# Kernel tuning notes

Hardware: AMD Instinct MI355X
Metric: run time of the kernel (lower is better)

Reference implementation:

```python
import jax, jax.numpy as jnp
import numpy as np

B, S, D = 1, 2048, 2048
H, KVH, HD = 32, 8, 64  # head_dim = D // H
THETA = 10000.0
INIT_STD = 0.02


def _freqs_cos_sin(head_dim, end, theta):
    # precompute_freqs_cis, returned as (cos, sin) real tables [end, head_dim//2]
    freqs = 1.0 / theta ** (np.arange(0, head_dim, 2)[: head_dim // 2].astype(np.float32) / head_dim)
    t = np.arange(end)
    fr = np.outer(t, freqs).astype(np.float32)
    return jnp.asarray(np.cos(fr)), jnp.asarray(np.sin(fr))


def setup_inputs() -> dict:
    key = jax.random.key(0)
    ks = jax.random.split(key, 5)
    return {
        "hidden_states": jax.random.normal(ks[0], (B, S, D), jnp.float32),
        "wq": jax.random.normal(ks[1], (D, H * HD), jnp.float32) * INIT_STD,
        "wk": jax.random.normal(ks[2], (D, KVH * HD), jnp.float32) * INIT_STD,
        "wv": jax.random.normal(ks[3], (D, KVH * HD), jnp.float32) * INIT_STD,
        "wo": jax.random.normal(ks[4], (H * HD, D), jnp.float32) * INIT_STD,
        "position_ids": jnp.broadcast_to(jnp.arange(S, dtype=jnp.int32), (B, S)),
    }


def reference(hidden_states, wq, wk, wv, wo, position_ids):
    # QKV projections (no bias)
    xq = (hidden_states @ wq).reshape(B, S, H, HD)
    xk = (hidden_states @ wk).reshape(B, S, KVH, HD)
    xv = (hidden_states @ wv).reshape(B, S, KVH, HD)

    # rotary embedding: interleaved complex pairs over last dim
    cos_t, sin_t = _freqs_cos_sin(HD, S, THETA)        # [S, HD//2]
    cos = cos_t[position_ids][:, :, None, :]            # [B, S, 1, HD//2]
    sin = sin_t[position_ids][:, :, None, :]

    def rope(x):
        xr = x.astype(jnp.float32).reshape(*x.shape[:-1], -1, 2)
        a, b = xr[..., 0], xr[..., 1]
        # (a + i b) * (cos + i sin)
        ra = a * cos - b * sin
        rb = a * sin + b * cos
        return jnp.stack((ra, rb), axis=-1).reshape(x.shape)

    xq = rope(xq)
    xk = rope(xk)

    # GQA: repeat kv heads
    n_rep = H // KVH
    xk = jnp.repeat(xk[:, :, :, None, :], n_rep, axis=3).reshape(B, S, H, HD)
    xv = jnp.repeat(xv[:, :, :, None, :], n_rep, axis=3).reshape(B, S, H, HD)

    # causal masked softmax attention (full score matrix, as in dot_product_attention_weights)
    scores = jnp.einsum('bqhd,bkhd->bhqk', xq, xk) / np.float32(np.sqrt(HD))
    causal = jnp.tril(jnp.ones((S, S), dtype=bool))
    big_neg = jnp.finfo(jnp.float32).min
    scores = jnp.where(causal[None, None, :, :], scores, big_neg)
    attn = jax.nn.softmax(scores, axis=-1)

    out = jnp.einsum('bhqk,bkhd->bqhd', attn, xv).reshape(B, S, H * HD)
    return out @ wo
```

## Files before the change

kernel.cpp:

```cpp
#include <hip/hip_runtime.h>
#include <hip/hip_bf16.h>


using short8  = __attribute__((ext_vector_type(8))) short;
using f32x4   = __attribute__((ext_vector_type(4))) float;
using f32x16  = __attribute__((ext_vector_type(16))) float;
using f32x2   = __attribute__((ext_vector_type(2))) float;
using ushort4v= __attribute__((ext_vector_type(4))) unsigned short;

#define SEQ 2048
#define DIM 2048
#define NH  32
#define NKVH 8
#define HD  64
#define KVD 512
#define NQKV 3072

#define GLOAD_LDS16(g, l) \
  __builtin_amdgcn_global_load_lds((const __attribute__((address_space(1))) void*)(g), \
                                   (__attribute__((address_space(3))) void*)(l), 16, 0, 0)

__device__ __forceinline__ float bf2f(unsigned short u) {
  union { float f; unsigned v; } x; x.v = ((unsigned)u) << 16; return x.f;
}
__device__ __forceinline__ unsigned short f2bf(float f) {
  union { float f; unsigned v; } x; x.f = f;
  unsigned r = x.v + 0x7fffu + ((x.v >> 16) & 1u);
  return (unsigned short)(r >> 16);
}

__global__ __launch_bounds__(256) void k_cast(const float* __restrict__ src,
                                              unsigned short* __restrict__ dst, int n) {
  int idx = (blockIdx.x * 256 + threadIdx.x) * 4;
  if (idx < n) {
    f32x4 v = *(const f32x4*)(src + idx);
    ushort4v o;
    o[0] = f2bf(v[0]); o[1] = f2bf(v[1]); o[2] = f2bf(v[2]); o[3] = f2bf(v[3]);
    *(ushort4v*)(dst + idx) = o;
  }
}

__global__ __launch_bounds__(256) void k_tcast(const float* __restrict__ src, int C,
                                               unsigned short* __restrict__ dst) {
  __shared__ float tile[32][33];
  int c0 = blockIdx.x * 32, r0 = blockIdx.y * 32;
  int tx = threadIdx.x, ty = threadIdx.y;
  #pragma unroll
  for (int j = 0; j < 32; j += 8)
    tile[ty + j][tx] = src[(r0 + ty + j) * C + c0 + tx];
  __syncthreads();
  #pragma unroll
  for (int j = 0; j < 32; j += 8)
    dst[(c0 + ty + j) * 2048 + r0 + tx] = f2bf(tile[tx][ty + j]);
}

__global__ __launch_bounds__(256) void k_table(const int* __restrict__ pos,
                                               f32x2* __restrict__ tab) {
  int i = blockIdx.x * 256 + threadIdx.x;
  int s = i >> 5, p = i & 31;
  float freq = powf(10000.0f, -(float)(2 * p) / 64.0f);
  float ang = (float)pos[s] * freq;
  float sv, cv; sincosf(ang, &sv, &cv);
  f32x2 r; r[0] = cv; r[1] = sv;
  tab[i] = r;
}

template <int N, bool OUTF32>
__global__ __launch_bounds__(256) void k_gemm(const unsigned short* __restrict__ A,
                                              const unsigned short* __restrict__ Bt,
                                              void* __restrict__ Cout) {
  const int K = 2048;
  __shared__ unsigned short lA[128 * 64];
  __shared__ unsigned short lB[128 * 64];
  int m0 = blockIdx.y * 128, n0 = blockIdx.x * 128;
  int t = threadIdx.x, lane = t & 63, wid = t >> 6;
  int wr = wid >> 1, wc = wid & 1;
  int lr = lane & 15, lg = lane >> 4;

  f32x4 acc[4][4] = {};

  for (int k0 = 0; k0 < K; k0 += 64) {
    #pragma unroll
    for (int j = 0; j < 4; ++j) {
      int idx = t + 256 * j, row = idx >> 3, c8 = idx & 7;
      GLOAD_LDS16(A  + (m0 + row) * K + k0 + c8 * 8, lA + idx * 8);
      GLOAD_LDS16(Bt + (n0 + row) * K + k0 + c8 * 8, lB + idx * 8);
    }
    __syncthreads();
    #pragma unroll
    for (int kk = 0; kk < 64; kk += 32) {
      short8 af[4], bfr[4];
      #pragma unroll
      for (int i = 0; i < 4; ++i) {
        af[i]  = *(const short8*)(lA + (wr * 64 + i * 16 + lr) * 64 + kk + lg * 8);
        bfr[i] = *(const short8*)(lB + (wc * 64 + i * 16 + lr) * 64 + kk + lg * 8);
      }
      #pragma unroll
      for (int i = 0; i < 4; ++i)
        #pragma unroll
        for (int j = 0; j < 4; ++j)
          acc[i][j] = __builtin_amdgcn_mfma_f32_16x16x32_bf16(af[i], bfr[j], acc[i][j], 0, 0, 0);
    }
    __syncthreads();
  }
  #pragma unroll
  for (int i = 0; i < 4; ++i)
    #pragma unroll
    for (int j = 0; j < 4; ++j)
      #pragma unroll
      for (int r = 0; r < 4; ++r) {
        int row = m0 + wr * 64 + i * 16 + lg * 4 + r;
        int col = n0 + wc * 64 + j * 16 + lr;
        float v = acc[i][j][r];
        if constexpr (OUTF32) ((float*)Cout)[row * N + col] = v;
        else ((unsigned short*)Cout)[row * N + col] = f2bf(v);
      }
}

__global__ __launch_bounds__(256) void k_rope(const unsigned short* __restrict__ xqkv,
                                              const f32x2* __restrict__ tab,
                                              unsigned short* __restrict__ xq,
                                              unsigned short* __restrict__ xk) {
  int s = blockIdx.y;
  int j = blockIdx.x * 256 + threadIdx.x;
  bool isq = j < 1024;
  int col = isq ? (2 * j) : (DIM + 2 * (j - 1024));
  int p = (col >> 1) & 31;
  f32x2 cs = tab[s * 32 + p];
  unsigned both = *(const unsigned*)(xqkv + s * NQKV + col);
  float a = bf2f((unsigned short)(both & 0xffff));
  float b = bf2f((unsigned short)(both >> 16));
  float ra = a * cs[0] - b * cs[1];
  float rb = a * cs[1] + b * cs[0];
  if (isq) { ra *= 0.125f; rb *= 0.125f; }
  unsigned pk = (unsigned)f2bf(ra) | ((unsigned)f2bf(rb) << 16);
  if (isq) *(unsigned*)(xq + s * DIM + col) = pk;
  else     *(unsigned*)(xk + s * KVD + (col - DIM)) = pk;
}

__global__ __launch_bounds__(256) void k_vt(const unsigned short* __restrict__ xqkv,
                                            unsigned short* __restrict__ xvT) {
  __shared__ unsigned short tile[32][33];
  int c0 = blockIdx.x * 32, s0 = blockIdx.y * 32;
  int tx = threadIdx.x, ty = threadIdx.y;
  #pragma unroll
  for (int j = 0; j < 32; j += 8)
    tile[ty + j][tx] = xqkv[(s0 + ty + j) * NQKV + 2560 + c0 + tx];
  __syncthreads();
  #pragma unroll
  for (int j = 0; j < 32; j += 8)
    xvT[(c0 + ty + j) * SEQ + s0 + tx] = tile[tx][ty + j];
}

__global__ __launch_bounds__(256) void k_attn(const unsigned short* __restrict__ xq,
                                              const unsigned short* __restrict__ xk,
                                              const unsigned short* __restrict__ xvT,
                                              unsigned short* __restrict__ attnout) {
  int wid = threadIdx.x >> 6, lane = threadIdx.x & 63;
  int tid = blockIdx.x * 4 + wid;
  int h = tid >> 5, j = tid & 31;
  int kvh = h >> 2;
  int lq = lane & 31, hi = lane >> 5;

  #pragma unroll
  for (int ph = 0; ph < 2; ++ph) {
    int qb = ph ? (63 - j) : j;
    int q0 = qb * 32;

    short8 qf[4];
    #pragma unroll
    for (int s = 0; s < 4; ++s)
      qf[s] = *(const short8*)(xq + (q0 + lq) * DIM + h * HD + s * 16 + hi * 8);

    f32x16 o0 = {}, o1 = {};
    float m = -3.0e38f, l = 0.0f;

    for (int kv0 = 0; kv0 <= q0; kv0 += 32) {
      f32x16 st = {};
      #pragma unroll
      for (int s = 0; s < 4; ++s) {
        short8 kf = *(const short8*)(xk + (kv0 + lq) * KVD + kvh * HD + s * 16 + hi * 8);
        st = __builtin_amdgcn_mfma_f32_32x32x16_bf16(kf, qf[s], st, 0, 0, 0);
      }
      if (kv0 == q0) {
        #pragma unroll
        for (int r = 0; r < 16; ++r) {
          int kvl = (r & 3) + 8 * (r >> 2) + 4 * hi;
          if (kvl > lq) st[r] = -3.0e38f;
        }
      }
      float pmax = st[0];
      #pragma unroll
      for (int r = 1; r < 16; ++r) pmax = fmaxf(pmax, st[r]);
      pmax = fmaxf(pmax, __shfl_xor(pmax, 32));
      if (!__all(pmax - m <= 8.0f)) {
        float mnew = fmaxf(m, pmax);
        float scale = __expf(m - mnew);
        #pragma unroll
        for (int r = 0; r < 16; ++r) {
          int ql = (r & 3) + 8 * (r >> 2) + 4 * hi;
          float sc = __shfl(scale, ql);
          o0[r] *= sc; o1[r] *= sc;
        }
        l *= scale;
        m = mnew;
      }
      float p[16], sum = 0.0f;
      #pragma unroll
      for (int r = 0; r < 16; ++r) { p[r] = __expf(st[r] - m); sum += p[r]; }
      l += sum;
      unsigned w[8];
      #pragma unroll
      for (int i = 0; i < 8; ++i)
        asm("v_cvt_pk_bf16_f32 %0, %1, %2" : "=v"(w[i]) : "v"(p[2 * i]), "v"(p[2 * i + 1]));
      #pragma unroll
      for (int s2 = 0; s2 < 2; ++s2) {
        int b = s2 * 4;
        unsigned sw0 = __shfl_xor(w[b + 0], 32);
        unsigned sw1 = __shfl_xor(w[b + 1], 32);
        unsigned sw2 = __shfl_xor(w[b + 2], 32);
        unsigned sw3 = __shfl_xor(w[b + 3], 32);
        union { unsigned u[4]; short8 s8; } pa;
        pa.u[0] = hi ? sw2 : w[b + 0];
        pa.u[1] = hi ? sw3 : w[b + 1];
        pa.u[2] = hi ? w[b + 2] : sw0;
        pa.u[3] = hi ? w[b + 3] : sw1;
        short8 v0 = *(const short8*)(xvT + (kvh * HD + lq)      * SEQ + kv0 + s2 * 16 + hi * 8);
        short8 v1 = *(const short8*)(xvT + (kvh * HD + 32 + lq) * SEQ + kv0 + s2 * 16 + hi * 8);
        o0 = __builtin_amdgcn_mfma_f32_32x32x16_bf16(pa.s8, v0, o0, 0, 0, 0);
        o1 = __builtin_amdgcn_mfma_f32_32x32x16_bf16(pa.s8, v1, o1, 0, 0, 0);
      }
    }
    float lt = l + __shfl_xor(l, 32);
    float linv = 1.0f / lt;
    #pragma unroll
    for (int r = 0; r < 16; ++r) {
      int ql = (r & 3) + 8 * (r >> 2) + 4 * hi;
      float li = __shfl(linv, ql);
      int row = q0 + ql;
      attnout[row * DIM + h * HD + lq]      = f2bf(o0[r] * li);
      attnout[row * DIM + h * HD + 32 + lq] = f2bf(o1[r] * li);
    }
  }
}

extern "C" void kernel_launch(void* const* d_in, const int* in_sizes, int n_in,
                              void* d_out, int out_size, void* d_ws, size_t ws_size,
                              hipStream_t stream) {
  const float* hs = (const float*)d_in[0];
  const float* wq = (const float*)d_in[1];
  const float* wk = (const float*)d_in[2];
  const float* wv = (const float*)d_in[3];
  const float* wo = (const float*)d_in[4];
  const int* pos  = (const int*)d_in[5];
  float* out = (float*)d_out;

  char* ws = (char*)d_ws;
  unsigned short* wqkvT = (unsigned short*)(ws);
  unsigned short* woT   = (unsigned short*)(ws + 12582912);
  unsigned short* hbf   = (unsigned short*)(ws + 20971520);
  unsigned short* xqkv  = (unsigned short*)(ws + 29360128);
  unsigned short* xq    = (unsigned short*)(ws + 41943040);
  unsigned short* xk    = (unsigned short*)(ws + 50331648);
  unsigned short* xvT   = (unsigned short*)(ws + 52428800);
  f32x2*          tab   = (f32x2*)(ws + 54525952);
  unsigned short* attnout = hbf;

  k_cast<<<4096, 256, 0, stream>>>(hs, hbf, SEQ * DIM);
  k_tcast<<<dim3(64, 64), dim3(32, 8), 0, stream>>>(wq, 2048, wqkvT);
  k_tcast<<<dim3(16, 64), dim3(32, 8), 0, stream>>>(wk, 512, wqkvT + 2048 * 2048);
  k_tcast<<<dim3(16, 64), dim3(32, 8), 0, stream>>>(wv, 512, wqkvT + 2560 * 2048);
  k_tcast<<<dim3(64, 64), dim3(32, 8), 0, stream>>>(wo, 2048, woT);
  k_table<<<256, 256, 0, stream>>>(pos, tab);

  k_gemm<NQKV, false><<<dim3(NQKV / 128, SEQ / 128), 256, 0, stream>>>(hbf, wqkvT, xqkv);

  k_rope<<<dim3(5, SEQ), 256, 0, stream>>>(xqkv, tab, xq, xk);
  k_vt<<<dim3(16, 64), dim3(32, 8), 0, stream>>>(xqkv, xvT);

  k_attn<<<256, 256, 0, stream>>>(xq, xk, xvT, attnout);

  k_gemm<DIM, true><<<dim3(DIM / 128, SEQ / 128), 256, 0, stream>>>(attnout, woT, out);
}
```

Measured before the change: 296.0 us.

## Split attention KV range across two wave halves and merge partial softmax states

The attention kernel now runs 512 threads per block. Each block holds the four query heads that share one KV head, and the causal KV range is split between two groups of waves, with the partial max, sum and output merged through shared memory. It also software-prefetches the next K/V tile into registers, raises wave priority around the MFMA sections, and folds log2(e) into the Q scale so the kernel can use exp2 directly. The intent is to double the waves per block to hide latency and shorten the critical path of long causal rows, at the cost of extra registers, shared-memory merge work and block-level syncs.

```diff
diff --git a/kernel.cpp b/kernel.cpp
--- a/kernel.cpp
+++ b/kernel.cpp
@@ -132,7 +132,8 @@
   float b = bf2f((unsigned short)(both >> 16));
   float ra = a * cs[0] - b * cs[1];
   float rb = a * cs[1] + b * cs[0];
-  if (isq) { ra *= 0.125f; rb *= 0.125f; }
+  const float QS = 0.125f * 1.44269504088896f;
+  if (isq) { ra *= QS; rb *= QS; }
   unsigned pk = (unsigned)f2bf(ra) | ((unsigned)f2bf(rb) << 16);
   if (isq) *(unsigned*)(xq + s * DIM + col) = pk;
   else     *(unsigned*)(xk + s * KVD + (col - DIM)) = pk;
@@ -152,20 +153,41 @@
     xvT[(c0 + ty + j) * SEQ + s0 + tx] = tile[tx][ty + j];
 }
 
-__global__ __launch_bounds__(256) void k_attn(const unsigned short* __restrict__ xq,
+__global__ __launch_bounds__(512) void k_attn(const unsigned short* __restrict__ xq,
                                               const unsigned short* __restrict__ xk,
                                               const unsigned short* __restrict__ xvT,
                                               unsigned short* __restrict__ attnout) {
+  __shared__ float obuf[4][64 * 36];
+  __shared__ float sm_m[4][2][32];
+  __shared__ float sm_l[4][32];
+
   int wid = threadIdx.x >> 6, lane = threadIdx.x & 63;
-  int tid = blockIdx.x * 4 + wid;
-  int h = tid >> 5, j = tid & 31;
-  int kvh = h >> 2;
+  int kvh = blockIdx.x & 7, j = blockIdx.x >> 3;
+  int h3 = wid & 3, half = wid >> 2;
+  int h = kvh * 4 + h3;
   int lq = lane & 31, hi = lane >> 5;
 
-  #pragma unroll
+  auto loadK = [&](int kv0, short8* d) {
+    #pragma unroll
+    for (int s = 0; s < 4; ++s)
+      d[s] = *(const short8*)(xk + (kv0 + lq) * KVD + kvh * HD + s * 16 + hi * 8);
+  };
+  auto loadV = [&](int kv0, short8* d) {
+    #pragma unroll
+    for (int s2 = 0; s2 < 2; ++s2) {
+      d[s2 * 2 + 0] = *(const short8*)(xvT + (kvh * HD + lq)      * SEQ + kv0 + s2 * 16 + hi * 8);
+      d[s2 * 2 + 1] = *(const short8*)(xvT + (kvh * HD + 32 + lq) * SEQ + kv0 + s2 * 16 + hi * 8);
+    }
+  };
+
+  #pragma unroll 1
   for (int ph = 0; ph < 2; ++ph) {
     int qb = ph ? (63 - j) : j;
     int q0 = qb * 32;
+    int T = qb + 1;
+    int c0 = (T + 1) >> 1;
+    int t0 = half ? c0 : 0;
+    int t1 = half ? T : c0;
 
     short8 qf[4];
     #pragma unroll
@@ -175,72 +197,110 @@
     f32x16 o0 = {}, o1 = {};
     float m = -3.0e38f, l = 0.0f;
 
-    for (int kv0 = 0; kv0 <= q0; kv0 += 32) {
-      f32x16 st = {};
-      #pragma unroll
-      for (int s = 0; s < 4; ++s) {
-        short8 kf = *(const short8*)(xk + (kv0 + lq) * KVD + kvh * HD + s * 16 + hi * 8);
-        st = __builtin_amdgcn_mfma_f32_32x32x16_bf16(kf, qf[s], st, 0, 0, 0);
-      }
-      if (kv0 == q0) {
-        #pragma unroll
-        for (int r = 0; r < 16; ++r) {
-          int kvl = (r & 3) + 8 * (r >> 2) + 4 * hi;
-          if (kvl > lq) st[r] = -3.0e38f;
+    if (t0 < t1) {
+      short8 kf[4], vf[4];
+      loadK(t0 * 32, kf); loadV(t0 * 32, vf);
+
+      for (int t = t0; t < t1; ++t) {
+        int kv0 = t * 32;
+        int kvn = min(t + 1, t1 - 1) * 32;
+        short8 kn[4], vn[4];
+        loadK(kvn, kn); loadV(kvn, vn);
+
+        f32x16 st = {};
+        __builtin_amdgcn_s_setprio(1);
+        #pragma unroll
+        for (int s = 0; s < 4; ++s)
+          st = __builtin_amdgcn_mfma_f32_32x32x16_bf16(kf[s], qf[s], st, 0, 0, 0);
+        __builtin_amdgcn_s_setprio(0);
+
+        if (kv0 == q0) {
+          #pragma unroll
+          for (int r = 0; r < 16; ++r) {
+            int kvl = (r & 3) + 8 * (r >> 2) + 4 * hi;
+            if (kvl > lq) st[r] = -3.0e38f;
+          }
         }
-      }
-      float pmax = st[0];
-      #pragma unroll
-      for (int r = 1; r < 16; ++r) pmax = fmaxf(pmax, st[r]);
-      pmax = fmaxf(pmax, __shfl_xor(pmax, 32));
-      if (!__all(pmax - m <= 8.0f)) {
-        float mnew = fmaxf(m, pmax);
-        float scale = __expf(m - mnew);
-        #pragma unroll
-        for (int r = 0; r < 16; ++r) {
-          int ql = (r & 3) + 8 * (r >> 2) + 4 * hi;
-          float sc = __shfl(scale, ql);
-          o0[r] *= sc; o1[r] *= sc;
+        float pmax = st[0];
+        #pragma unroll
+        for (int r = 1; r < 16; ++r) pmax = fmaxf(pmax, st[r]);
+        pmax = fmaxf(pmax, __shfl_xor(pmax, 32));
+        if (!__all(pmax - m <= 11.54f)) {
+          float mnew = fmaxf(m, pmax);
+          float scale = exp2f(m - mnew);
+          #pragma unroll
+          for (int r = 0; r < 16; ++r) {
+            int ql = (r & 3) + 8 * (r >> 2) + 4 * hi;
+            float sc = __shfl(scale, ql);
+            o0[r] *= sc; o1[r] *= sc;
+          }
+          l *= scale;
+          m = mnew;
         }
-        l *= scale;
-        m = mnew;
-      }
-      float p[16], sum = 0.0f;
-      #pragma unroll
-      for (int r = 0; r < 16; ++r) { p[r] = __expf(st[r] - m); sum += p[r]; }
-      l += sum;
-      unsigned w[8];
-      #pragma unroll
-      for (int i = 0; i < 8; ++i)
-        asm("v_cvt_pk_bf16_f32 %0, %1, %2" : "=v"(w[i]) : "v"(p[2 * i]), "v"(p[2 * i + 1]));
-      #pragma unroll
-      for (int s2 = 0; s2 < 2; ++s2) {
-        int b = s2 * 4;
-        unsigned sw0 = __shfl_xor(w[b + 0], 32);
-        unsigned sw1 = __shfl_xor(w[b + 1], 32);
-        unsigned sw2 = __shfl_xor(w[b + 2], 32);
-        unsigned sw3 = __shfl_xor(w[b + 3], 32);
-        union { unsigned u[4]; short8 s8; } pa;
-        pa.u[0] = hi ? sw2 : w[b + 0];
-        pa.u[1] = hi ? sw3 : w[b + 1];
-        pa.u[2] = hi ? w[b + 2] : sw0;
-        pa.u[3] = hi ? w[b + 3] : sw1;
-        short8 v0 = *(const short8*)(xvT + (kvh * HD + lq)      * SEQ + kv0 + s2 * 16 + hi * 8);
-        short8 v1 = *(const short8*)(xvT + (kvh * HD + 32 + lq) * SEQ + kv0 + s2 * 16 + hi * 8);
-        o0 = __builtin_amdgcn_mfma_f32_32x32x16_bf16(pa.s8, v0, o0, 0, 0, 0);
-        o1 = __builtin_amdgcn_mfma_f32_32x32x16_bf16(pa.s8, v1, o1, 0, 0, 0);
-      }
-    }
-    float lt = l + __shfl_xor(l, 32);
-    float linv = 1.0f / lt;
-    #pragma unroll
-    for (int r = 0; r < 16; ++r) {
-      int ql = (r & 3) + 8 * (r >> 2) + 4 * hi;
-      float li = __shfl(linv, ql);
-      int row = q0 + ql;
-      attnout[row * DIM + h * HD + lq]      = f2bf(o0[r] * li);
-      attnout[row * DIM + h * HD + 32 + lq] = f2bf(o1[r] * li);
-    }
+        float p[16], sum = 0.0f;
+        #pragma unroll
+        for (int r = 0; r < 16; ++r) { p[r] = exp2f(st[r] - m); sum += p[r]; }
+        l += sum;
+        unsigned w[8];
+        #pragma unroll
+        for (int i = 0; i < 8; ++i)
+          asm("v_cvt_pk_bf16_f32 %0, %1, %2" : "=v"(w[i]) : "v"(p[2 * i]), "v"(p[2 * i + 1]));
+        __builtin_amdgcn_s_setprio(1);
+        #pragma unroll
+        for (int s2 = 0; s2 < 2; ++s2) {
+          int b = s2 * 4;
+          unsigned sw0 = __shfl_xor(w[b + 0], 32);
+          unsigned sw1 = __shfl_xor(w[b + 1], 32);
+          unsigned sw2 = __shfl_xor(w[b + 2], 32);
+          unsigned sw3 = __shfl_xor(w[b + 3], 32);
+          union { unsigned u[4]; short8 s8; } pa;
+          pa.u[0] = hi ? sw2 : w[b + 0];
+          pa.u[1] = hi ? sw3 : w[b + 1];
+          pa.u[2] = hi ? w[b + 2] : sw0;
+          pa.u[3] = hi ? w[b + 3] : sw1;
+          o0 = __builtin_amdgcn_mfma_f32_32x32x16_bf16(pa.s8, vf[s2 * 2 + 0], o0, 0, 0, 0);
+          o1 = __builtin_amdgcn_mfma_f32_32x32x16_bf16(pa.s8, vf[s2 * 2 + 1], o1, 0, 0, 0);
+        }
+        __builtin_amdgcn_s_setprio(0);
+        #pragma unroll
+        for (int s = 0; s < 4; ++s) { kf[s] = kn[s]; vf[s] = vn[s]; }
+      }
+    }
+
+    float lc = l + __shfl_xor(l, 32);
+    if (hi == 0) sm_m[h3][half][lq] = m;
+    __syncthreads();
+    float mo = sm_m[h3][half ^ 1][lq];
+    float mstar = fmaxf(m, mo);
+    float s = exp2f(m - mstar);
+    if (half) {
+      if (hi == 0) sm_l[h3][lq] = lc * s;
+      float* ob = &obuf[h3][lane * 36];
+      #pragma unroll
+      for (int r = 0; r < 16; ++r) {
+        int ql = (r & 3) + 8 * (r >> 2) + 4 * hi;
+        float sc = __shfl(s, ql);
+        ob[r] = o0[r] * sc;
+        ob[16 + r] = o1[r] * sc;
+      }
+    }
+    __syncthreads();
+    if (!half) {
+      float lB = sm_l[h3][lq];
+      float ltot = lc * s + lB;
+      float linv = 1.0f / ltot;
+      const float* ob = &obuf[h3][lane * 36];
+      #pragma unroll
+      for (int r = 0; r < 16; ++r) {
+        int ql = (r & 3) + 8 * (r >> 2) + 4 * hi;
+        float sc = __shfl(s, ql);
+        float li = __shfl(linv, ql);
+        int row = q0 + ql;
+        attnout[row * DIM + h * HD + lq]      = f2bf((o0[r] * sc + ob[r]) * li);
+        attnout[row * DIM + h * HD + 32 + lq] = f2bf((o1[r] * sc + ob[16 + r]) * li);
+      }
+    }
+    if (ph == 0) __syncthreads();
   }
 }
 
@@ -278,7 +338,7 @@
   k_rope<<<dim3(5, SEQ), 256, 0, stream>>>(xqkv, tab, xq, xk);
   k_vt<<<dim3(16, 64), dim3(32, 8), 0, stream>>>(xqkv, xvT);
 
-  k_attn<<<256, 256, 0, stream>>>(xq, xk, xvT, attnout);
+  k_attn<<<256, 512, 0, stream>>>(xq, xk, xvT, attnout);
 
   k_gemm<DIM, true><<<dim3(DIM / 128, SEQ / 128), 256, 0, stream>>>(attnout, woT, out);
 }
```

Result: faster. 282.6 us (-4.5%).
